# Kernel optimization log

Hardware: AMD Instinct MI355X
Metric: run time of the kernel (lower is better)

Reference implementation:

```python
import jax, jax.numpy as jnp
import numpy as np

NUM_USERS = 100000
NUM_ITEMS = 50000
N_NODES = NUM_USERS + NUM_ITEMS
LATENT_DIM = 64
N_LAYERS = 3
NNZ = 2400000
BATCH = 16384


def setup_inputs() -> dict:
    key = jax.random.key(0)
    k1, k2, k3, k4, k5, k6, k7 = jax.random.split(key, 7)
    user_emb = jax.random.normal(k1, (NUM_USERS, LATENT_DIM), dtype=jnp.float32) * 0.1
    item_emb = jax.random.normal(k2, (NUM_ITEMS, LATENT_DIM), dtype=jnp.float32) * 0.1
    edge_rows = jax.random.randint(k3, (NNZ,), 0, N_NODES, dtype=jnp.int32)
    edge_cols = jax.random.randint(k4, (NNZ,), 0, N_NODES, dtype=jnp.int32)
    # normalized-adjacency-like positive weights
    edge_vals = jax.random.uniform(k5, (NNZ,), dtype=jnp.float32) * 0.05
    user_input = jax.random.randint(k6, (BATCH,), 0, NUM_USERS, dtype=jnp.int64)
    item_input = jax.random.randint(k7, (BATCH,), 0, NUM_ITEMS, dtype=jnp.int64)
    return {
        "user_emb": user_emb,
        "item_emb": item_emb,
        "edge_rows": edge_rows,
        "edge_cols": edge_cols,
        "edge_vals": edge_vals,
        "user_input": user_input,
        "item_input": item_input,
    }


def _spmm(edge_rows, edge_cols, edge_vals, x):
    # sparse [N,N] @ dense [N,D] via gather + weighted segment-sum
    gathered = x[edge_cols] * edge_vals[:, None]  # [nnz, D]
    return jax.ops.segment_sum(gathered, edge_rows, num_segments=N_NODES)


def reference(user_emb, item_emb, edge_rows, edge_cols, edge_vals, user_input, item_input):
    all_emb = jnp.concatenate([user_emb, item_emb], axis=0)  # [N, D]
    acc = all_emb
    for _ in range(N_LAYERS):
        all_emb = _spmm(edge_rows, edge_cols, edge_vals, all_emb)
        acc = acc + all_emb
    light_out = acc / (N_LAYERS + 1)  # mean over stacked layer embeddings
    users_avg = light_out[:NUM_USERS]
    items_avg = light_out[NUM_USERS:]
    u = users_avg[user_input]  # [B, D]
    i = items_avg[item_input]  # [B, D]
    preds = jnp.sum(u * i, axis=1)  # [B]
    return preds
```

## Files before the change

kernel.cpp:

```cpp
#include <hip/hip_runtime.h>

#define NUM_USERS 100000
#define NUM_ITEMS 50000
#define N_NODES   150000
#define DIM       64
#define BATCH_N   16384
#define NPART     586
#define NBUCK     8
#define SC_SLICE  18750

__global__ __launch_bounds__(256) void lg_hist(const int* __restrict__ rows,
                                               int* __restrict__ cnt, int nnz) {
    int e = blockIdx.x * blockDim.x + threadIdx.x;
    if (e < nnz) atomicAdd(&cnt[rows[e]], 1);
}

__global__ __launch_bounds__(256) void lg_scan1(const int* __restrict__ cnt,
                                                int* __restrict__ ptr,
                                                int* __restrict__ part) {
    __shared__ int s[256];
    int i = blockIdx.x * 256 + threadIdx.x;
    int v = (i < N_NODES) ? cnt[i] : 0;
    s[threadIdx.x] = v;
    __syncthreads();
    #pragma unroll
    for (int off = 1; off < 256; off <<= 1) {
        int t = (threadIdx.x >= off) ? s[threadIdx.x - off] : 0;
        __syncthreads();
        s[threadIdx.x] += t;
        __syncthreads();
    }
    if (i < N_NODES) ptr[i] = s[threadIdx.x] - v;
    if (threadIdx.x == 255) part[blockIdx.x] = s[255];
}

__global__ __launch_bounds__(64) void lg_scan2(int* __restrict__ part, int n) {
    int lane = threadIdx.x & 63;
    int run = 0;
    for (int base = 0; base < n; base += 64) {
        int i = base + lane;
        int v = (i < n) ? part[i] : 0;
        int orig = v;
        #pragma unroll
        for (int off = 1; off < 64; off <<= 1) {
            int t = __shfl_up(v, off, 64);
            if (lane >= off) v += t;
        }
        if (i < n) part[i] = run + v - orig;
        run += __shfl(v, 63, 64);
    }
}

__global__ __launch_bounds__(256) void lg_scan3(int* __restrict__ ptr,
                                                const int* __restrict__ part,
                                                int* __restrict__ cur) {
    int i = blockIdx.x * 256 + threadIdx.x;
    if (i < N_NODES) {
        int p = ptr[i] + part[blockIdx.x];
        ptr[i] = p;
        cur[i] = p;
    }
}

__global__ void lg_bcur(const int* __restrict__ ptr, int* __restrict__ bcur) {
    int t = threadIdx.x;
    if (t < NBUCK) bcur[t] = ptr[t * SC_SLICE];
}

__global__ __launch_bounds__(256) void lg_bucket(const int* __restrict__ rows,
                           const int* __restrict__ cols,
                           const float* __restrict__ vals,
                           int* __restrict__ bcur,
                           int* __restrict__ brow, int2* __restrict__ bcv, int nnz) {
    __shared__ int hist[NBUCK], base[NBUCK], off[NBUCK];
    if (threadIdx.x < NBUCK) { hist[threadIdx.x] = 0; off[threadIdx.x] = 0; }
    __syncthreads();
    int e = blockIdx.x * 256 + threadIdx.x;
    int r = 0, b = -1;
    if (e < nnz) { r = rows[e]; b = r / SC_SLICE; atomicAdd(&hist[b], 1); }
    __syncthreads();
    if (threadIdx.x < NBUCK && hist[threadIdx.x] > 0)
        base[threadIdx.x] = atomicAdd(&bcur[threadIdx.x], hist[threadIdx.x]);
    __syncthreads();
    if (b >= 0) {
        int rank = atomicAdd(&off[b], 1);
        int pos  = base[b] + rank;
        brow[pos] = r;
        bcv[pos]  = make_int2(cols[e], __float_as_int(vals[e]));
    }
}

__global__ __launch_bounds__(256) void lg_scatter2(const int* __restrict__ brow,
                           const int2* __restrict__ bcv,
                           const int* __restrict__ ptr, int* __restrict__ cur,
                           int2* __restrict__ edges, int b, int nnz) {
    int lo = __builtin_amdgcn_readfirstlane(ptr[b * SC_SLICE]);
    int hi = (b == NBUCK - 1) ? nnz
             : __builtin_amdgcn_readfirstlane(ptr[(b + 1) * SC_SLICE]);
    int i = lo + blockIdx.x * 256 + threadIdx.x;
    if (i >= hi) return;
    int r = brow[i];
    int pos = atomicAdd(&cur[r], 1);
    edges[pos] = bcv[i];
}

__global__ __launch_bounds__(256) void lg_spmm(const int* __restrict__ ptr,
                            const int* __restrict__ cnt,
                            const int2* __restrict__ edges,
                            const float* __restrict__ xu,
                            const float* __restrict__ xi,
                            float* __restrict__ yout) {
    int r    = blockIdx.x * 4 + (threadIdx.x >> 6);
    int lane = threadIdx.x & 63;
    if (r >= N_NODES) return;
    int start = __builtin_amdgcn_readfirstlane(ptr[r]);
    int len   = __builtin_amdgcn_readfirstlane(cnt[r]);
    const int2* __restrict__ ep = edges + start;
    float s0 = 0.0f, s1 = 0.0f, s2 = 0.0f, s3 = 0.0f;
    int j = 0;
    for (; j + 8 <= len; j += 8) {
        int2 m0 = ep[j];     int2 m1 = ep[j + 1];
        int2 m2 = ep[j + 2]; int2 m3 = ep[j + 3];
        int2 m4 = ep[j + 4]; int2 m5 = ep[j + 5];
        int2 m6 = ep[j + 6]; int2 m7 = ep[j + 7];
        const float* b0 = (m0.x < NUM_USERS) ? xu : xi;
        const float* b1 = (m1.x < NUM_USERS) ? xu : xi;
        const float* b2 = (m2.x < NUM_USERS) ? xu : xi;
        const float* b3 = (m3.x < NUM_USERS) ? xu : xi;
        const float* b4 = (m4.x < NUM_USERS) ? xu : xi;
        const float* b5 = (m5.x < NUM_USERS) ? xu : xi;
        const float* b6 = (m6.x < NUM_USERS) ? xu : xi;
        const float* b7 = (m7.x < NUM_USERS) ? xu : xi;
        s0 += __int_as_float(m0.y) * b0[(m0.x << 6) + lane];
        s1 += __int_as_float(m1.y) * b1[(m1.x << 6) + lane];
        s2 += __int_as_float(m2.y) * b2[(m2.x << 6) + lane];
        s3 += __int_as_float(m3.y) * b3[(m3.x << 6) + lane];
        s0 += __int_as_float(m4.y) * b4[(m4.x << 6) + lane];
        s1 += __int_as_float(m5.y) * b5[(m5.x << 6) + lane];
        s2 += __int_as_float(m6.y) * b6[(m6.x << 6) + lane];
        s3 += __int_as_float(m7.y) * b7[(m7.x << 6) + lane];
    }
    for (; j < len; ++j) {
        int2 m = ep[j];
        const float* b = (m.x < NUM_USERS) ? xu : xi;
        s0 += __int_as_float(m.y) * b[(m.x << 6) + lane];
    }
    float sum = (s0 + s1) + (s2 + s3);
    yout[(r << 6) + lane] = sum;
}

__global__ __launch_bounds__(256) void lg_dot4(const float* __restrict__ ue,
                       const float* __restrict__ ie,
                       const float* __restrict__ x1,
                       const float* __restrict__ x2,
                       const float* __restrict__ x3,
                       const int*   __restrict__ uidx,
                       const int*   __restrict__ iidx,
                       float*       __restrict__ out,
                       int batch) {
    int bb   = blockIdx.x * 4 + (threadIdx.x >> 6);
    int lane = threadIdx.x & 63;
    if (bb >= batch) return;
    int u = uidx[bb];
    int i = iidx[bb];
    int t = NUM_USERS + i;
    int uo = (u << 6) + lane;
    int to = (t << 6) + lane;
    float au = ue[(u << 6) + lane] + x1[uo] + x2[uo] + x3[uo];
    float at = ie[(i << 6) + lane] + x1[to] + x2[to] + x3[to];
    float p  = au * at * (1.0f / 16.0f);
    #pragma unroll
    for (int off = 32; off > 0; off >>= 1)
        p += __shfl_down(p, off, 64);
    if (lane == 0) out[bb] = p;
}

extern "C" void kernel_launch(void* const* d_in, const int* in_sizes, int n_in,
                              void* d_out, int out_size, void* d_ws, size_t ws_size,
                              hipStream_t stream) {
    const float* user_emb  = (const float*)d_in[0];
    const float* item_emb  = (const float*)d_in[1];
    const int*   edge_rows = (const int*)  d_in[2];
    const int*   edge_cols = (const int*)  d_in[3];
    const float* edge_vals = (const float*)d_in[4];
    const int*   user_inp  = (const int*)  d_in[5];
    const int*   item_inp  = (const int*)  d_in[6];
    float*       out       = (float*)d_out;

    const int nnz = in_sizes[2];

    const size_t embBytes = (size_t)N_NODES * DIM * sizeof(float);
    const size_t nodeInts = (size_t)N_NODES * sizeof(int);
    const size_t need = 3 * embBytes + (size_t)nnz * 8 + 3 * nodeInts
                      + (size_t)(NPART + NBUCK) * sizeof(int);
    if (ws_size < need) return;

    char* ws = (char*)d_ws;
    float* x1    = (float*)(ws);
    float* x2    = (float*)(ws + embBytes);
    float* x3    = (float*)(ws + 2 * embBytes);
    int2*  edges = (int2*) (ws + 3 * embBytes);
    int*   cnt   = (int*)  (ws + 3 * embBytes + (size_t)nnz * 8);
    int*   ptr   = (int*)  (ws + 3 * embBytes + (size_t)nnz * 8 + nodeInts);
    int*   cur   = (int*)  (ws + 3 * embBytes + (size_t)nnz * 8 + 2 * nodeInts);
    int*   part  = (int*)  (ws + 3 * embBytes + (size_t)nnz * 8 + 3 * nodeInts);
    int*   bcur  = part + NPART;
    int*   brow  = (int*)x1;
    int2*  bcv   = (int2*)((char*)x1 + (size_t)nnz * 4);

    hipMemsetAsync(cnt, 0, nodeInts, stream);
    const int eb = (nnz + 255) / 256;
    lg_hist <<<eb,    256, 0, stream>>>(edge_rows, cnt, nnz);
    lg_scan1<<<NPART, 256, 0, stream>>>(cnt, ptr, part);
    lg_scan2<<<1,      64, 0, stream>>>(part, NPART);
    lg_scan3<<<NPART, 256, 0, stream>>>(ptr, part, cur);
    lg_bcur <<<1,      64, 0, stream>>>(ptr, bcur);
    lg_bucket<<<eb,   256, 0, stream>>>(edge_rows, edge_cols, edge_vals,
                                        bcur, brow, bcv, nnz);
    const int sgrid = (nnz / NBUCK + nnz / 64 + 255) / 256;
    for (int b = 0; b < NBUCK; ++b)
        lg_scatter2<<<sgrid, 256, 0, stream>>>(brow, bcv, ptr, cur, edges, b, nnz);

    const int rowBlocks = (N_NODES + 3) / 4;
    const float* xi_shift = item_emb - (size_t)NUM_USERS * DIM;
    lg_spmm<<<rowBlocks, 256, 0, stream>>>(ptr, cnt, edges, user_emb, xi_shift, x1);
    lg_spmm<<<rowBlocks, 256, 0, stream>>>(ptr, cnt, edges, x1, x1, x2);
    lg_spmm<<<rowBlocks, 256, 0, stream>>>(ptr, cnt, edges, x2, x2, x3);

    lg_dot4<<<(BATCH_N + 3) / 4, 256, 0, stream>>>(user_emb, item_emb, x1, x2, x3,
                                                   user_inp, item_inp, out, BATCH_N);
}
```

Baseline: 740.7 us.

## Replace bucket pre-pass with row-range filtered scatter passes over raw edges

Drops the bucketing kernel and its bcur setup. Each of 8 scatter passes now reads the full original rows array, filters to its row slice, and reads cols/vals only for matching edges to write into CSR order. This removes one full write and re-read of the bucketed intermediate arrays, but every pass rescans all row indices, so the rows array is read eight times. The SpMM remainder loop is also replaced with 4/2/1 unrolled tail steps to expose more memory-level parallelism.

After: 617.6 us. -16.6%, faster.

```diff
diff --git a/kernel.cpp b/kernel.cpp
--- a/kernel.cpp
+++ b/kernel.cpp
@@ -6,7 +6,7 @@
 #define DIM       64
 #define BATCH_N   16384
 #define NPART     586
-#define NBUCK     8
+#define SC_PASSES 8
 #define SC_SLICE  18750
 
 __global__ __launch_bounds__(256) void lg_hist(const int* __restrict__ rows,
@@ -62,46 +62,16 @@
     }
 }
 
-__global__ void lg_bcur(const int* __restrict__ ptr, int* __restrict__ bcur) {
-    int t = threadIdx.x;
-    if (t < NBUCK) bcur[t] = ptr[t * SC_SLICE];
-}
-
-__global__ __launch_bounds__(256) void lg_bucket(const int* __restrict__ rows,
+__global__ __launch_bounds__(256) void lg_scatter_pass(const int* __restrict__ rows,
                            const int* __restrict__ cols,
-                           const float* __restrict__ vals,
-                           int* __restrict__ bcur,
-                           int* __restrict__ brow, int2* __restrict__ bcv, int nnz) {
-    __shared__ int hist[NBUCK], base[NBUCK], off[NBUCK];
-    if (threadIdx.x < NBUCK) { hist[threadIdx.x] = 0; off[threadIdx.x] = 0; }
-    __syncthreads();
-    int e = blockIdx.x * 256 + threadIdx.x;
-    int r = 0, b = -1;
-    if (e < nnz) { r = rows[e]; b = r / SC_SLICE; atomicAdd(&hist[b], 1); }
-    __syncthreads();
-    if (threadIdx.x < NBUCK && hist[threadIdx.x] > 0)
-        base[threadIdx.x] = atomicAdd(&bcur[threadIdx.x], hist[threadIdx.x]);
-    __syncthreads();
-    if (b >= 0) {
-        int rank = atomicAdd(&off[b], 1);
-        int pos  = base[b] + rank;
-        brow[pos] = r;
-        bcv[pos]  = make_int2(cols[e], __float_as_int(vals[e]));
-    }
-}
-
-__global__ __launch_bounds__(256) void lg_scatter2(const int* __restrict__ brow,
-                           const int2* __restrict__ bcv,
-                           const int* __restrict__ ptr, int* __restrict__ cur,
-                           int2* __restrict__ edges, int b, int nnz) {
-    int lo = __builtin_amdgcn_readfirstlane(ptr[b * SC_SLICE]);
-    int hi = (b == NBUCK - 1) ? nnz
-             : __builtin_amdgcn_readfirstlane(ptr[(b + 1) * SC_SLICE]);
-    int i = lo + blockIdx.x * 256 + threadIdx.x;
-    if (i >= hi) return;
-    int r = brow[i];
+                           const float* __restrict__ vals, int* __restrict__ cur,
+                           int2* __restrict__ edges, int nnz, int lo, int hi) {
+    int e = blockIdx.x * blockDim.x + threadIdx.x;
+    if (e >= nnz) return;
+    int r = rows[e];
+    if (r < lo || r >= hi) return;
     int pos = atomicAdd(&cur[r], 1);
-    edges[pos] = bcv[i];
+    edges[pos] = make_int2(cols[e], __float_as_int(vals[e]));
 }
 
 __global__ __launch_bounds__(256) void lg_spmm(const int* __restrict__ ptr,
@@ -140,7 +110,28 @@
         s2 += __int_as_float(m6.y) * b6[(m6.x << 6) + lane];
         s3 += __int_as_float(m7.y) * b7[(m7.x << 6) + lane];
     }
-    for (; j < len; ++j) {
+    if (j + 4 <= len) {
+        int2 m0 = ep[j];     int2 m1 = ep[j + 1];
+        int2 m2 = ep[j + 2]; int2 m3 = ep[j + 3];
+        const float* b0 = (m0.x < NUM_USERS) ? xu : xi;
+        const float* b1 = (m1.x < NUM_USERS) ? xu : xi;
+        const float* b2 = (m2.x < NUM_USERS) ? xu : xi;
+        const float* b3 = (m3.x < NUM_USERS) ? xu : xi;
+        s0 += __int_as_float(m0.y) * b0[(m0.x << 6) + lane];
+        s1 += __int_as_float(m1.y) * b1[(m1.x << 6) + lane];
+        s2 += __int_as_float(m2.y) * b2[(m2.x << 6) + lane];
+        s3 += __int_as_float(m3.y) * b3[(m3.x << 6) + lane];
+        j += 4;
+    }
+    if (j + 2 <= len) {
+        int2 m0 = ep[j];     int2 m1 = ep[j + 1];
+        const float* b0 = (m0.x < NUM_USERS) ? xu : xi;
+        const float* b1 = (m1.x < NUM_USERS) ? xu : xi;
+        s0 += __int_as_float(m0.y) * b0[(m0.x << 6) + lane];
+        s1 += __int_as_float(m1.y) * b1[(m1.x << 6) + lane];
+        j += 2;
+    }
+    if (j < len) {
         int2 m = ep[j];
         const float* b = (m.x < NUM_USERS) ? xu : xi;
         s0 += __int_as_float(m.y) * b[(m.x << 6) + lane];
@@ -192,7 +183,7 @@
     const size_t embBytes = (size_t)N_NODES * DIM * sizeof(float);
     const size_t nodeInts = (size_t)N_NODES * sizeof(int);
     const size_t need = 3 * embBytes + (size_t)nnz * 8 + 3 * nodeInts
-                      + (size_t)(NPART + NBUCK) * sizeof(int);
+                      + (size_t)NPART * sizeof(int);
     if (ws_size < need) return;
 
     char* ws = (char*)d_ws;
@@ -204,9 +195,6 @@
     int*   ptr   = (int*)  (ws + 3 * embBytes + (size_t)nnz * 8 + nodeInts);
     int*   cur   = (int*)  (ws + 3 * embBytes + (size_t)nnz * 8 + 2 * nodeInts);
     int*   part  = (int*)  (ws + 3 * embBytes + (size_t)nnz * 8 + 3 * nodeInts);
-    int*   bcur  = part + NPART;
-    int*   brow  = (int*)x1;
-    int2*  bcv   = (int2*)((char*)x1 + (size_t)nnz * 4);
 
     hipMemsetAsync(cnt, 0, nodeInts, stream);
     const int eb = (nnz + 255) / 256;
@@ -214,12 +202,10 @@
     lg_scan1<<<NPART, 256, 0, stream>>>(cnt, ptr, part);
     lg_scan2<<<1,      64, 0, stream>>>(part, NPART);
     lg_scan3<<<NPART, 256, 0, stream>>>(ptr, part, cur);
-    lg_bcur <<<1,      64, 0, stream>>>(ptr, bcur);
-    lg_bucket<<<eb,   256, 0, stream>>>(edge_rows, edge_cols, edge_vals,
-                                        bcur, brow, bcv, nnz);
-    const int sgrid = (nnz / NBUCK + nnz / 64 + 255) / 256;
-    for (int b = 0; b < NBUCK; ++b)
-        lg_scatter2<<<sgrid, 256, 0, stream>>>(brow, bcv, ptr, cur, edges, b, nnz);
+    for (int p = 0; p < SC_PASSES; ++p)
+        lg_scatter_pass<<<eb, 256, 0, stream>>>(edge_rows, edge_cols, edge_vals,
+                                                cur, edges, nnz,
+                                                p * SC_SLICE, (p + 1) * SC_SLICE);
 
     const int rowBlocks = (N_NODES + 3) / 4;
     const float* xi_shift = item_emb - (size_t)NUM_USERS * DIM;
```
